# Optimization experiments

Measured on AMD Instinct MI355X. Metric: run time of the kernel, lower is better.

The kernel has to match this reference:

```python
import jax, jax.numpy as jnp
import numpy as np

N_NODES = 50000


def _gcn_conv(x, row, col, W, b, n_nodes):
    """PyG GCNConv: symmetric-normalized scatter-add aggregation.
    row/col already include self-loops. x: [N, Fin], W: [Fin, Fout]."""
    h = x @ W  # [N, Fout]
    deg = jax.ops.segment_sum(jnp.ones(col.shape[0], x.dtype), col,
                              num_segments=n_nodes)  # in-degree incl. self-loops
    dis = jnp.where(deg > 0, jax.lax.rsqrt(deg), 0.0)  # deg^{-1/2}
    norm = dis[row] * dis[col]  # [E+N]
    msg = h[row] * norm[:, None]  # gather + scale, [E+N, Fout]
    out = jax.ops.segment_sum(msg, col, num_segments=n_nodes)  # scatter-add
    return out + b


def setup_inputs() -> dict:
    key = jax.random.key(0)
    k1, k2, k3, k4 = jax.random.split(key, 4)
    N, E, FIN, FH = N_NODES, 800000, 512, 512
    x = jax.random.normal(k1, (N, FIN), dtype=jnp.float32)
    edge_index = jax.random.randint(k2, (2, E), 0, N, dtype=jnp.int64)
    W1 = jax.random.normal(k3, (FIN, FH), dtype=jnp.float32) * (1.0 / np.sqrt(FIN))
    b1 = jnp.zeros((FH,), jnp.float32)
    W2 = jax.random.normal(k4, (FH, FH), dtype=jnp.float32) * (1.0 / np.sqrt(FH))
    b2 = jnp.zeros((FH,), jnp.float32)
    return {"x": x, "edge_index": edge_index, "W1": W1, "b1": b1,
            "W2": W2, "b2": b2}


def reference(x, edge_index, W1, b1, W2, b2):
    n = x.shape[0]
    loops = jnp.arange(n, dtype=edge_index.dtype)
    row = jnp.concatenate([edge_index[0], loops])  # sources
    col = jnp.concatenate([edge_index[1], loops])  # targets
    h = _gcn_conv(x, row, col, W1, b1, n)
    h = jax.nn.relu(h)
    return _gcn_conv(h, row, col, W2, b2, n)
```

## Files before the change

### kernel.cpp

```cpp
#include <hip/hip_runtime.h>
#include <hip/hip_bf16.h>

typedef short short8 __attribute__((ext_vector_type(8)));
typedef unsigned short u16x8 __attribute__((ext_vector_type(8)));
typedef float f32x4 __attribute__((ext_vector_type(4)));

#define AS1 __attribute__((address_space(1)))
#define AS3 __attribute__((address_space(3)))

__device__ __forceinline__ void gload16(const void* g, void* l) {
  __builtin_amdgcn_global_load_lds((AS1 void*)g, (AS3 void*)l, 16, 0, 0);
}

__device__ __forceinline__ unsigned short f2bf(float f) {
  unsigned u = __float_as_uint(f);
  u = (u + 0x7FFF + ((u >> 16) & 1)) >> 16;
  return (unsigned short)u;
}
__device__ __forceinline__ float bf2f(unsigned short u) {
  return __uint_as_float(((unsigned)u) << 16);
}

__global__ void prep_kernel(const float4* __restrict__ x4, ushort4* __restrict__ xb4, int n4,
                            const float* __restrict__ W1, unsigned short* __restrict__ W1t,
                            const float* __restrict__ W2, unsigned short* __restrict__ W2t) {
  const int nthr = gridDim.x * 256;
  for (int i = blockIdx.x * 256 + threadIdx.x; i < n4; i += nthr) {
    float4 v = x4[i];
    ushort4 o;
    o.x = f2bf(v.x); o.y = f2bf(v.y); o.z = f2bf(v.z); o.w = f2bf(v.w);
    xb4[i] = o;
  }
  for (int idx = blockIdx.x * 256 + threadIdx.x; idx < 512 * 512; idx += nthr) {
    const int k = idx >> 9, n = idx & 511;
    W1t[n * 512 + k] = f2bf(W1[idx]);
    W2t[n * 512 + k] = f2bf(W2[idx]);
  }
}

__global__ void detect64_kernel(const int* __restrict__ ei32, int* __restrict__ flag) {
  const int lane = threadIdx.x;
  const int v = ei32[2 * lane + 1];
  const unsigned long long m = __ballot(v != 0);
  if (lane == 0) *flag = (m == 0ull) ? 1 : 0;
}

__global__ void count_kernel(const int* __restrict__ ei32, const int* __restrict__ flag,
                             int* __restrict__ cnt4, int E, int qdiv) {
  int e = blockIdx.x * 256 + threadIdx.x;
  if (e >= E) return;
  const int is64 = *flag;
  const int r = is64 ? ei32[2 * e] : ei32[e];
  const int c = is64 ? ei32[2 * E + 2 * e] : ei32[E + e];
  int q = r / qdiv; q = q > 3 ? 3 : q;
  atomicAdd(&cnt4[c * 4 + q], 1);
}

__global__ void __launch_bounds__(1024) scan_bsum_kernel(const int* __restrict__ cnt,
                                                         int* __restrict__ bsum, int n) {
  __shared__ int ws[16];
  const int tid = threadIdx.x, lane = tid & 63, wid = tid >> 6;
  const int i = blockIdx.x * 1024 + tid;
  int x = (i < n) ? cnt[i] : 0;
#pragma unroll
  for (int d = 1; d < 64; d <<= 1) x += __shfl_xor(x, d, 64);
  if (lane == 0) ws[wid] = x;
  __syncthreads();
  if (tid == 0) {
    int s = 0;
#pragma unroll
    for (int w = 0; w < 16; ++w) s += ws[w];
    bsum[blockIdx.x] = s;
  }
}

__global__ void __launch_bounds__(1024) scan_boff_kernel(int* __restrict__ bsum,
                                                         int* __restrict__ total, int B) {
  __shared__ int ws[16];
  const int tid = threadIdx.x, lane = tid & 63, wid = tid >> 6;
  const int v = (tid < B) ? bsum[tid] : 0;
  int x = v;
#pragma unroll
  for (int d = 1; d < 64; d <<= 1) {
    int y = __shfl_up(x, d, 64);
    if (lane >= d) x += y;
  }
  if (lane == 63) ws[wid] = x;
  __syncthreads();
  if (tid < 16) {
    int wv = ws[tid];
    int wx = wv;
#pragma unroll
    for (int d = 1; d < 16; d <<= 1) {
      int y = __shfl_up(wx, d, 64);
      if (tid >= d) wx += y;
    }
    ws[tid] = wx - wv;
  }
  __syncthreads();
  const int excl = ws[wid] + (x - v);
  if (tid < B) bsum[tid] = excl;
  if (tid == B - 1) *total = excl + v;
}

__global__ void __launch_bounds__(1024) scan_fill_kernel(const int* __restrict__ cnt,
    const int* __restrict__ boff, int* __restrict__ ptr, int* __restrict__ cur,
    float* __restrict__ dis, int n) {
  __shared__ int ws[16];
  const int tid = threadIdx.x, lane = tid & 63, wid = tid >> 6;
  const int j = blockIdx.x * 1024 + tid;
  const int v = (j < n) ? cnt[j] : 0;
  int x = v;
#pragma unroll
  for (int d = 1; d < 64; d <<= 1) {
    int y = __shfl_up(x, d, 64);
    if (lane >= d) x += y;
  }
  if (lane == 63) ws[wid] = x;
  __syncthreads();
  if (tid < 16) {
    int wv = ws[tid];
    int wx = wv;
#pragma unroll
    for (int d = 1; d < 16; d <<= 1) {
      int y = __shfl_up(wx, d, 64);
      if (tid >= d) wx += y;
    }
    ws[tid] = wx - wv;
  }
  __syncthreads();
  const int v1 = __shfl_down(v, 1, 64);
  const int v2 = __shfl_down(v, 2, 64);
  const int v3 = __shfl_down(v, 3, 64);
  if (j < n) {
    const int excl = boff[blockIdx.x] + ws[wid] + (x - v);
    ptr[j] = excl;
    cur[j] = excl;
    if ((j & 3) == 0) dis[j >> 2] = rsqrtf((float)(v + v1 + v2 + v3 + 1));
  }
}

__global__ void fill_kernel(const int* __restrict__ ei32, const int* __restrict__ flag,
                            int* __restrict__ cur4, int* __restrict__ eidx, int E, int qdiv) {
  int e = blockIdx.x * 256 + threadIdx.x;
  if (e >= E) return;
  const int is64 = *flag;
  const int r = is64 ? ei32[2 * e] : ei32[e];
  const int c = is64 ? ei32[2 * E + 2 * e] : ei32[E + e];
  int q = r / qdiv; q = q > 3 ? 3 : q;
  const int pos = atomicAdd(&cur4[c * 4 + q], 1);
  eidx[pos] = r;
}

template <bool BA, bool BC>
__global__ void __launch_bounds__(256) gemm_kernel(const unsigned short* __restrict__ A,
                                                   const unsigned short* __restrict__ Bt,
                                                   const float* __restrict__ dscale,
                                                   unsigned short* __restrict__ C, int M) {
  __shared__ alignas(128) unsigned short As[2][8192];
  __shared__ alignas(128) unsigned short Bs[2][8192];
  const int tid = threadIdx.x;
  const int wave = tid >> 6, lane = tid & 63;
  const int wm = wave >> 1, wn = wave & 1;

  const int nbm = (M + 127) >> 7;
  const int nwg = nbm * 4;
  const int orig = blockIdx.x;
  const int xcd = orig & 7;
  const int q8 = nwg >> 3, r8 = nwg & 7;
  const int wg = (xcd < r8 ? xcd * (q8 + 1) : r8 * (q8 + 1) + (xcd - r8) * q8) + (orig >> 3);
  const int bn = wg & 3;
  const int bm = wg >> 2;

  const int lr = lane >> 3, ls = lane & 7;
  const int fr = lane & 15, ks = lane >> 4;

  f32x4 acc[4][4] = {};

#define STAGE(BUF, KO)                                                                     \
  {                                                                                        \
    _Pragma("unroll") for (int i = 0; i < 4; ++i) {                                        \
      int ra = bm * 128 + i * 32 + wave * 8 + lr;                                          \
      ra = ra < M ? ra : M - 1;                                                            \
      const size_t aoff = BA ? ((size_t)(KO)*M + (size_t)ra * 64 + ((ls ^ (lr & 7)) << 3)) \
                             : ((size_t)ra * 512 + (KO) + ((ls ^ (lr & 7)) << 3));         \
      gload16(A + aoff, &As[BUF][(i * 32 + wave * 8) * 64]);                               \
      const int rb = bn * 128 + i * 32 + wave * 8 + lr;                                    \
      gload16(Bt + (size_t)rb * 512 + (KO) + ((ls ^ (lr & 7)) << 3),                       \
              &Bs[BUF][(i * 32 + wave * 8) * 64]);                                         \
    }                                                                                      \
  }

  STAGE(0, 0)
  __syncthreads();

  int buf = 0;
  for (int kt = 0; kt < 8; ++kt) {
    if (kt < 7) STAGE(buf ^ 1, (kt + 1) * 64)

    short8 af[2][4], bfg[2][4];
#pragma unroll
    for (int m = 0; m < 4; ++m) {
      const int tr = wm * 64 + m * 16 + fr;
      af[0][m] = *(const short8*)&As[buf][tr * 64 + (((ks * 8)      ) ^ ((tr & 7) << 3))];
      af[1][m] = *(const short8*)&As[buf][tr * 64 + (((ks * 8) + 32 ) ^ ((tr & 7) << 3))];
    }
#pragma unroll
    for (int n = 0; n < 4; ++n) {
      const int tb = wn * 64 + n * 16 + fr;
      bfg[0][n] = *(const short8*)&Bs[buf][tb * 64 + (((ks * 8)      ) ^ ((tb & 7) << 3))];
      bfg[1][n] = *(const short8*)&Bs[buf][tb * 64 + (((ks * 8) + 32 ) ^ ((tb & 7) << 3))];
    }
#pragma unroll
    for (int kk = 0; kk < 2; ++kk)
#pragma unroll
      for (int m = 0; m < 4; ++m)
#pragma unroll
        for (int n = 0; n < 4; ++n)
          acc[m][n] = __builtin_amdgcn_mfma_f32_16x16x32_bf16(af[kk][m], bfg[kk][n], acc[m][n], 0, 0, 0);

    __syncthreads();
    buf ^= 1;
  }
#undef STAGE

  const int rbase = bm * 128 + wm * 64 + (lane >> 4) * 4;
  const int cbase = bn * 128 + wn * 64 + (lane & 15);
  const size_t hseg = (size_t)M * 64;
#pragma unroll
  for (int m = 0; m < 4; ++m)
#pragma unroll
    for (int j = 0; j < 4; ++j) {
      const int r = rbase + m * 16 + j;
      if (r < M) {
        const float ds = dscale[r];
#pragma unroll
        for (int n = 0; n < 4; ++n) {
          const unsigned short val = f2bf(acc[m][n][j] * ds);
          if (BC) {
            const int col = cbase + n * 16;
            C[(size_t)(col >> 6) * hseg + (size_t)r * 64 + (col & 63)] = val;
          } else {
            C[(size_t)r * 512 + cbase + n * 16] = val;
          }
        }
      }
    }
}

template <bool FINAL>
__global__ void __launch_bounds__(256) agg_kernel(const unsigned short* __restrict__ h,
    const int* __restrict__ eidx, const int* __restrict__ ptr4, const float* __restrict__ dis,
    const float* __restrict__ bias, void* __restrict__ outv, int n) {
  const int tid = threadIdx.x;
  const int lane = tid & 63;
  const int slice = blockIdx.x & 7;
  const int g = lane >> 3;
  const int c = lane & 7;
  const int node = (int)(blockIdx.x >> 3) * 32 + (tid >> 6) * 8 + g;
  if (node >= n) return;

  const unsigned short* hs = h + (size_t)slice * ((size_t)n * 64);
  const int coff = c * 8;

  const int start = ptr4[node * 4], end = ptr4[node * 4 + 4];
  float acc[8] = {0, 0, 0, 0, 0, 0, 0, 0};

  int e = start;
  for (; e + 2 <= end; e += 2) {
    const int s0 = eidx[e], s1 = eidx[e + 1];
    const u16x8 v0 = *(const u16x8*)(hs + (size_t)(unsigned)s0 * 64 + coff);
    const u16x8 v1 = *(const u16x8*)(hs + (size_t)(unsigned)s1 * 64 + coff);
#pragma unroll
    for (int j = 0; j < 8; ++j) acc[j] += bf2f(v0[j]) + bf2f(v1[j]);
  }
  if (e < end) {
    const int s0 = eidx[e];
    const u16x8 v = *(const u16x8*)(hs + (size_t)(unsigned)s0 * 64 + coff);
#pragma unroll
    for (int j = 0; j < 8; ++j) acc[j] += bf2f(v[j]);
  }

  {
    const u16x8 v = *(const u16x8*)(hs + (size_t)node * 64 + coff);
#pragma unroll
    for (int j = 0; j < 8; ++j) acc[j] += bf2f(v[j]);
  }

  const float di = dis[node];
  const int fcol = slice * 64 + coff;
  float b[8];
  *(float4*)&b[0] = *(const float4*)(bias + fcol);
  *(float4*)&b[4] = *(const float4*)(bias + fcol + 4);

  if (FINAL) {
    float* out = (float*)outv;
    float4 o0, o1;
    o0.x = acc[0] * di + b[0]; o0.y = acc[1] * di + b[1];
    o0.z = acc[2] * di + b[2]; o0.w = acc[3] * di + b[3];
    o1.x = acc[4] * di + b[4]; o1.y = acc[5] * di + b[5];
    o1.z = acc[6] * di + b[6]; o1.w = acc[7] * di + b[7];
    *(float4*)(out + (size_t)node * 512 + fcol) = o0;
    *(float4*)(out + (size_t)node * 512 + fcol + 4) = o1;
  } else {
    unsigned short* out = (unsigned short*)outv;
    u16x8 o;
#pragma unroll
    for (int j = 0; j < 8; ++j) {
      const float t = acc[j] * di + b[j];
      o[j] = f2bf(t > 0.0f ? t : 0.0f);
    }
    *(u16x8*)(out + (size_t)slice * ((size_t)n * 64) + (size_t)node * 64 + coff) = o;
  }
}

extern "C" void kernel_launch(void* const* d_in, const int* in_sizes, int n_in,
                              void* d_out, int out_size, void* d_ws, size_t ws_size,
                              hipStream_t stream) {
  const float* x  = (const float*)d_in[0];
  const int*   ei = (const int*)d_in[1];
  const float* W1 = (const float*)d_in[2];
  const float* b1 = (const float*)d_in[3];
  const float* W2 = (const float*)d_in[4];
  const float* b2 = (const float*)d_in[5];
  float* out = (float*)d_out;

  const int M = in_sizes[0] / 512;
  const int E = in_sizes[1] / 2;
  const int qdiv = (M + 3) >> 2;

  auto alignup = [](size_t v) { return (v + 255) & ~(size_t)255; };
  char* p = (char*)d_ws;
  unsigned short* xb  = (unsigned short*)p; p += alignup((size_t)M * 512 * 2);
  unsigned short* h1b = (unsigned short*)p; p += alignup((size_t)M * 512 * 2);
  unsigned short* r1b = (unsigned short*)p; p += alignup((size_t)M * 512 * 2);
  unsigned short* w1b = (unsigned short*)p; p += alignup(512 * 512 * 2);
  unsigned short* w2b = (unsigned short*)p; p += alignup(512 * 512 * 2);
  float* dis = (float*)p; p += alignup((size_t)M * 4);
  int* ptr4  = (int*)p;   p += alignup(((size_t)M * 4 + 1) * 4);
  int* eidx  = (int*)p;   p += alignup((size_t)E * 4);
  int* flag  = (int*)p;   p += alignup(256);
  int* bsum  = (int*)p;   p += alignup(1024);
  int* cnt4 = (int*)h1b;
  int* cur4 = (int*)((char*)h1b + alignup((size_t)M * 16));
  unsigned short* h2b = xb;

  const int n4 = M * 4;
  hipMemsetAsync(cnt4, 0, (size_t)n4 * 4, stream);
  detect64_kernel<<<1, 64, 0, stream>>>(ei, flag);

  prep_kernel<<<2048, 256, 0, stream>>>((const float4*)x, (ushort4*)xb, M * 128,
                                        W1, w1b, W2, w2b);

  const int B = (n4 + 1023) / 1024;
  count_kernel<<<(E + 255) / 256, 256, 0, stream>>>(ei, flag, cnt4, E, qdiv);
  scan_bsum_kernel<<<B, 1024, 0, stream>>>(cnt4, bsum, n4);
  scan_boff_kernel<<<1, 1024, 0, stream>>>(bsum, ptr4 + n4, B);
  scan_fill_kernel<<<B, 1024, 0, stream>>>(cnt4, bsum, ptr4, cur4, dis, n4);
  fill_kernel<<<(E + 255) / 256, 256, 0, stream>>>(ei, flag, cur4, eidx, E, qdiv);

  const int nwg = ((M + 127) / 128) * 4;
  const int nag = ((M + 31) / 32) * 8;
  gemm_kernel<false, true><<<nwg, 256, 0, stream>>>(xb, w1b, dis, h1b, M);
  agg_kernel<false><<<nag, 256, 0, stream>>>(h1b, eidx, ptr4, dis, b1, (void*)r1b, M);
  gemm_kernel<true, true><<<nwg, 256, 0, stream>>>(r1b, w2b, dis, h2b, M);
  agg_kernel<true><<<nag, 256, 0, stream>>>(h2b, eidx, ptr4, dis, b2, (void*)out, M);
}
```

Before: 404.8 us.

## Single-buffer GEMM LDS tiles and raise occupancy with launch bounds

Drops the LDS double-buffering in the bf16 MFMA GEMM, halving shared memory per block to 32KB, and adds a min-blocks-per-CU hint of 3. Fragment registers are now loaded per k-half to cut register pressure. The aim is to hide latency through more resident workgroups rather than software prefetch. The cost is that global-to-LDS loads no longer overlap compute within a block, and there is an extra barrier per k-step.

After: 380.3 us. 6.0% less time.

```diff
diff --git a/kernel.cpp b/kernel.cpp
--- a/kernel.cpp
+++ b/kernel.cpp
@@ -153,12 +153,12 @@
 }
 
 template <bool BA, bool BC>
-__global__ void __launch_bounds__(256) gemm_kernel(const unsigned short* __restrict__ A,
-                                                   const unsigned short* __restrict__ Bt,
-                                                   const float* __restrict__ dscale,
-                                                   unsigned short* __restrict__ C, int M) {
-  __shared__ alignas(128) unsigned short As[2][8192];
-  __shared__ alignas(128) unsigned short Bs[2][8192];
+__global__ void __launch_bounds__(256, 3) gemm_kernel(const unsigned short* __restrict__ A,
+                                                      const unsigned short* __restrict__ Bt,
+                                                      const float* __restrict__ dscale,
+                                                      unsigned short* __restrict__ C, int M) {
+  __shared__ alignas(128) unsigned short As[8192];
+  __shared__ alignas(128) unsigned short Bs[8192];
   const int tid = threadIdx.x;
   const int wave = tid >> 6, lane = tid & 63;
   const int wm = wave >> 1, wn = wave & 1;
@@ -177,50 +177,44 @@
 
   f32x4 acc[4][4] = {};
 
-#define STAGE(BUF, KO)                                                                     \
+#define STAGE(KO)                                                                          \
   {                                                                                        \
     _Pragma("unroll") for (int i = 0; i < 4; ++i) {                                        \
       int ra = bm * 128 + i * 32 + wave * 8 + lr;                                          \
       ra = ra < M ? ra : M - 1;                                                            \
       const size_t aoff = BA ? ((size_t)(KO)*M + (size_t)ra * 64 + ((ls ^ (lr & 7)) << 3)) \
                              : ((size_t)ra * 512 + (KO) + ((ls ^ (lr & 7)) << 3));         \
-      gload16(A + aoff, &As[BUF][(i * 32 + wave * 8) * 64]);                               \
+      gload16(A + aoff, &As[(i * 32 + wave * 8) * 64]);                                    \
       const int rb = bn * 128 + i * 32 + wave * 8 + lr;                                    \
       gload16(Bt + (size_t)rb * 512 + (KO) + ((ls ^ (lr & 7)) << 3),                       \
-              &Bs[BUF][(i * 32 + wave * 8) * 64]);                                         \
+              &Bs[(i * 32 + wave * 8) * 64]);                                              \
     }                                                                                      \
   }
 
-  STAGE(0, 0)
-  __syncthreads();
-
-  int buf = 0;
   for (int kt = 0; kt < 8; ++kt) {
-    if (kt < 7) STAGE(buf ^ 1, (kt + 1) * 64)
-
-    short8 af[2][4], bfg[2][4];
-#pragma unroll
-    for (int m = 0; m < 4; ++m) {
-      const int tr = wm * 64 + m * 16 + fr;
-      af[0][m] = *(const short8*)&As[buf][tr * 64 + (((ks * 8)      ) ^ ((tr & 7) << 3))];
-      af[1][m] = *(const short8*)&As[buf][tr * 64 + (((ks * 8) + 32 ) ^ ((tr & 7) << 3))];
-    }
-#pragma unroll
-    for (int n = 0; n < 4; ++n) {
-      const int tb = wn * 64 + n * 16 + fr;
-      bfg[0][n] = *(const short8*)&Bs[buf][tb * 64 + (((ks * 8)      ) ^ ((tb & 7) << 3))];
-      bfg[1][n] = *(const short8*)&Bs[buf][tb * 64 + (((ks * 8) + 32 ) ^ ((tb & 7) << 3))];
-    }
-#pragma unroll
-    for (int kk = 0; kk < 2; ++kk)
+    if (kt) __syncthreads();
+    STAGE(kt * 64)
+    __syncthreads();
+
+#pragma unroll
+    for (int kk = 0; kk < 2; ++kk) {
+      short8 af[4], bfg[4];
+#pragma unroll
+      for (int m = 0; m < 4; ++m) {
+        const int tr = wm * 64 + m * 16 + fr;
+        af[m] = *(const short8*)&As[tr * 64 + ((ks * 8 + kk * 32) ^ ((tr & 7) << 3))];
+      }
+#pragma unroll
+      for (int n = 0; n < 4; ++n) {
+        const int tb = wn * 64 + n * 16 + fr;
+        bfg[n] = *(const short8*)&Bs[tb * 64 + ((ks * 8 + kk * 32) ^ ((tb & 7) << 3))];
+      }
 #pragma unroll
       for (int m = 0; m < 4; ++m)
 #pragma unroll
         for (int n = 0; n < 4; ++n)
-          acc[m][n] = __builtin_amdgcn_mfma_f32_16x16x32_bf16(af[kk][m], bfg[kk][n], acc[m][n], 0, 0, 0);
-
-    __syncthreads();
-    buf ^= 1;
+          acc[m][n] = __builtin_amdgcn_mfma_f32_16x16x32_bf16(af[m], bfg[n], acc[m][n], 0, 0, 0);
+    }
   }
 #undef STAGE
 
```
